# Optimization experiments

Hardware: AMD Instinct MI355X
Metric: run time of the kernel (lower is better)

Reference implementation:

```python
import jax, jax.numpy as jnp
import numpy as np

K_TOP = 2          # hardcoded k in MyAttentionFunction
S = 32             # hardcoded spatial size (interpolate to 32x32)
N = S * S          # 1024 patches (patch_size=1, stride=1 unfold)
NEG = jnp.float32(-1e30)  # stand-in for excluding columns from top-k


def setup_inputs() -> dict:
    key = jax.random.key(0)
    k1, k2, k3 = jax.random.split(key, 3)
    C = 4096
    generated = jax.random.normal(k1, (1, C, S, S), dtype=jnp.float32)
    known = jax.random.normal(k2, (1, C, S, S), dtype=jnp.float32)
    mask = jax.random.randint(k3, (1, 1, S, S), 0, 2).astype(jnp.float32)
    return {"generated": generated, "known": known, "mask": mask}


def _forward(generated, known, mask):
    C = generated.shape[1]
    # F.interpolate(mask, (32,32)) nearest, then flatten -> flag in {0,1}, shape (N,)
    flag = jax.image.resize(mask, (1, 1, S, S), method="nearest").reshape(N)
    # MyUnfold(x, 1, 1) == [1, N, C]; drop batch dim of 1.
    P = generated.reshape(C, N).T   # (N, C) patches of `generated`
    Kp = known.reshape(C, N).T      # (N, C) patches of `known`

    norm_p = jnp.sum(P * P, axis=-1)   # (N,)
    norm_k = jnp.sum(Kp * Kp, axis=-1)
    # Full cosine matrices; original restricts rows to flag==1 and columns to
    # flag==0 (cosine0) / flag==1 (cosine1) by extraction; we mask columns with
    # a very negative value so top-k returns the same values with GLOBAL indices
    # (which is exactly what the original reconstructs via nonzero()[indexes]).
    cos0 = (P @ Kp.T) / jnp.sqrt(norm_p[:, None] * norm_k[None, :])  # (N, N)
    cos1 = (P @ P.T) / jnp.sqrt(norm_p[:, None] * norm_p[None, :])
    cos0 = jnp.where(flag[None, :] == 0, cos0, NEG)
    cos1 = jnp.where(flag[None, :] == 1, cos1, NEG)

    w0, i0 = jax.lax.top_k(cos0, K_TOP)  # (N, k) values / global indices
    w1, i1 = jax.lax.top_k(cos1, K_TOP)

    m = flag                      # 1.0 on masked rows
    nm = jnp.sum(m)               # number of masked patches
    # weight means taken only over masked rows, then softmax (original uses
    # .item() + numpy softmax, i.e. detached constants).
    means = jnp.stack(
        [jnp.sum(w0[:, i] * m) / nm for i in range(K_TOP)]
        + [jnp.sum(w1[:, i] * m) / nm for i in range(K_TOP)]
    )
    weights = jax.lax.stop_gradient(jax.nn.softmax(means))  # (2k,)

    # The original builds dense 1024x1024 indicator matrices and bmm's them;
    # each indicator row for a masked patch is one-hot at its retrieved source,
    # so the bmm is just a gather into masked rows. The advanced-indexing quirk
    # ind[mask_idx, src_idx] (nonzero() pairs include a leading 0 column) also
    # unconditionally sets ind[0,0]=1; we reproduce that (set semantics: no
    # double count if row 0 already maps to column 0).
    rtn = jnp.zeros((N, C), dtype=generated.dtype)
    for i in range(2 * K_TOP):
        src = Kp if i < K_TOP else P
        cols = (i0 if i < K_TOP else i1)[:, i % K_TOP]  # (N,) global indices
        out_i = jnp.where(m[:, None] == 1, src[cols], 0.0)  # masked rows only
        dup = 1.0 - ((m[0] == 1) & (cols[0] == 0)).astype(src.dtype)
        out_i = out_i.at[0].add(src[0] * dup)  # spurious ind[0,0]=1 artifact
        rtn = rtn + weights[i] * out_i

    rtn = rtn.reshape(1, S, S, C).transpose(0, 3, 1, 2)  # (1, C, 32, 32)
    return jnp.concatenate([generated, known, rtn], axis=1)


def reference(generated, known, mask):
    return _forward(generated, known, mask)
```

## Files before the change

### kernel.cpp

```cpp
#include <hip/hip_runtime.h>
#include <hip/hip_bf16.h>
#include <math.h>

#define N_TOT 1024
#define C_DIM 4096
#define T_MARGIN 3e-4f

typedef __attribute__((ext_vector_type(8))) _Float16 half8;
typedef __attribute__((ext_vector_type(8))) unsigned short ushort8;
typedef __attribute__((ext_vector_type(8))) char schar8;
typedef __attribute__((ext_vector_type(4))) float floatx4;

__device__ inline unsigned short f2h(float v) {
    _Float16 h = (_Float16)v;
    return __builtin_bit_cast(unsigned short, h);
}
__device__ inline float h2f(unsigned short u) {
    return (float)__builtin_bit_cast(_Float16, u);
}
__device__ inline char lo_enc(float v, unsigned short h) {
    int e = (h >> 10) & 31;
    float lo = v - h2f(h);
    float q = rintf(lo * 240.0f * __uint_as_float((unsigned)(152 - e) << 23));
    q = fmaxf(-127.0f, fminf(127.0f, q));
    return (char)(int)q;
}
__device__ inline float lo_dec(char q, unsigned short h) {
    int e = (h >> 10) & 31;
    return (float)q * __uint_as_float((unsigned)(e + 102) << 23) * (1.0f / 240.0f);
}

__device__ inline void ins2(float v, int s, float& v1, int& s1, float& v2, int& s2) {
    if (v > v1 || (v == v1 && s < s1)) { v2 = v1; s2 = s1; v1 = v; s1 = s; }
    else if (v > v2 || (v == v2 && s < s2)) { v2 = v; s2 = s; }
}

__global__ __launch_bounds__(256) void split_norms(const float* __restrict__ G,
                                                   const float* __restrict__ Kn,
                                                   const float* __restrict__ flag,
                                                   unsigned short* __restrict__ Phi,
                                                   char* __restrict__ Plo,
                                                   unsigned short* __restrict__ Khi,
                                                   char* __restrict__ Klo,
                                                   float* __restrict__ normP,
                                                   float* __restrict__ normK,
                                                   int* __restrict__ colidx,
                                                   int* __restrict__ n0p) {
    const int z = blockIdx.z;
    const float* X = z ? Kn : G;
    unsigned short* Xhi = z ? Khi : Phi;
    char* Xlo = z ? Klo : Plo;
    float* normX = z ? normK : normP;

    __shared__ float tile[64 * 65];
    __shared__ float np[256];
    const int t  = threadIdx.x;
    const int c0 = blockIdx.x * 64;
    const int n0 = blockIdx.y * 64;

    float s2 = 0.0f;
    #pragma unroll
    for (int s = 0; s < 16; s++) {
        int c_loc = s * 4 + (t >> 6);
        int n_loc = t & 63;
        float v = X[(c0 + c_loc) * N_TOT + n0 + n_loc];
        tile[c_loc * 65 + n_loc] = v;
        s2 = fmaf(v, v, s2);
    }
    np[t] = s2;
    __syncthreads();

    if (t < 64) {
        float tot = np[t] + np[t + 64] + np[t + 128] + np[t + 192];
        atomicAdd(&normX[n0 + t], tot);
    }

    #pragma unroll
    for (int s = 0; s < 4; s++) {
        int n_loc = s * 16 + (t >> 4);
        int c4    = (t & 15) * 4;
        unsigned short h[4]; char l[4];
        #pragma unroll
        for (int e = 0; e < 4; e++) {
            float v = tile[(c4 + e) * 65 + n_loc];
            h[e] = f2h(v);
            l[e] = lo_enc(v, h[e]);
        }
        size_t base = (size_t)(n0 + n_loc) * C_DIM + c0 + c4;
        *(ushort4*)&Xhi[base] = make_ushort4(h[0], h[1], h[2], h[3]);
        *(char4*)&Xlo[base]   = make_char4(l[0], l[1], l[2], l[3]);
    }

    if (blockIdx.x == 0 && blockIdx.y == 0 && blockIdx.z == 0) {
        __shared__ int cz[256];
        __shared__ int co[256];
        float4 fv = *(const float4*)&flag[4 * t];
        int f[4] = {fv.x == 0.0f, fv.y == 0.0f, fv.z == 0.0f, fv.w == 0.0f};
        int nz = f[0] + f[1] + f[2] + f[3];
        cz[t] = nz; co[t] = 4 - nz;
        __syncthreads();
        for (int off = 1; off < 256; off <<= 1) {
            int vz = (t >= off) ? cz[t - off] : 0;
            int vo = (t >= off) ? co[t - off] : 0;
            __syncthreads();
            cz[t] += vz; co[t] += vo;
            __syncthreads();
        }
        const int fn0 = cz[255];
        int zs = cz[t] - nz;
        int os = fn0 + co[t] - (4 - nz);
        #pragma unroll
        for (int e = 0; e < 4; e++) {
            int j = 4 * t + e;
            if (f[e]) colidx[zs++] = j;
            else      colidx[os++] = j;
        }
        if (t == 0) *n0p = fn0;
    }
}

__global__ __launch_bounds__(256, 4) void gemm_coarse(const unsigned short* __restrict__ Phi,
                                                      const unsigned short* __restrict__ Khi,
                                                      const int* __restrict__ colidx,
                                                      const int* __restrict__ n0p,
                                                      float* __restrict__ dotPart) {
    __shared__ unsigned short sA[64 * 64];
    __shared__ unsigned short sB[128 * 64];

    const int t    = threadIdx.x;
    const int wave = t >> 6, lane = t & 63;
    const int wm   = wave >> 1, wn = wave & 1;
    const int quad = lane >> 4, lrow = lane & 15;
    const int ib = blockIdx.x * 64, jb = blockIdx.y * 128;
    const int bz = blockIdx.z;
    const int k_beg = bz * 512;
    const int n0 = *n0p;

    const int srow = t >> 3;
    const int g    = (t & 7) ^ (srow & 7);

    const unsigned short* gA[2];
    gA[0] = Phi + (size_t)(ib + srow) * C_DIM + g * 8;
    gA[1] = gA[0] + (size_t)32 * C_DIM;
    const unsigned short* gB[4];
    #pragma unroll
    for (int q = 0; q < 4; q++) {
        int s = jb + q * 32 + srow;
        int row = colidx[s];
        const unsigned short* src = (s < n0) ? Khi : Phi;
        gB[q] = src + (size_t)row * C_DIM + g * 8;
    }

    floatx4 acc[2][4] = {};

    for (int k0 = k_beg; k0 < k_beg + 512; k0 += 64) {
        #pragma unroll
        for (int q = 0; q < 2; q++)
            __builtin_amdgcn_global_load_lds(
                (const __attribute__((address_space(1))) void*)(gA[q] + k0),
                (__attribute__((address_space(3))) void*)((char*)sA + q * 4096 + t * 16), 16, 0, 0);
        #pragma unroll
        for (int q = 0; q < 4; q++)
            __builtin_amdgcn_global_load_lds(
                (const __attribute__((address_space(1))) void*)(gB[q] + k0),
                (__attribute__((address_space(3))) void*)((char*)sB + q * 4096 + t * 16), 16, 0, 0);
        __syncthreads();

        #pragma unroll
        for (int kk = 0; kk < 2; kk++) {
            const int gk = kk * 4 + quad;
            half8 a[2], b[4];
            #pragma unroll
            for (int ti = 0; ti < 2; ti++) {
                int m = wm * 32 + ti * 16 + lrow;
                a[ti] = *(const half8*)&sA[m * 64 + ((gk ^ (m & 7)) << 3)];
            }
            #pragma unroll
            for (int tj = 0; tj < 4; tj++) {
                int n = wn * 64 + tj * 16 + lrow;
                b[tj] = *(const half8*)&sB[n * 64 + ((gk ^ (n & 7)) << 3)];
            }
            #pragma unroll
            for (int ti = 0; ti < 2; ti++)
                #pragma unroll
                for (int tj = 0; tj < 4; tj++)
                    acc[ti][tj] = __builtin_amdgcn_mfma_f32_16x16x32_f16(a[ti], b[tj], acc[ti][tj], 0, 0, 0);
        }
        __syncthreads();
    }

    float* outp = dotPart + ((size_t)bz << 20);
    #pragma unroll
    for (int tj = 0; tj < 4; tj++) {
        int j = jb + wn * 64 + tj * 16 + lrow;
        #pragma unroll
        for (int ti = 0; ti < 2; ti++) {
            #pragma unroll
            for (int reg = 0; reg < 4; reg++) {
                int i = ib + wm * 32 + ti * 16 + quad * 4 + reg;
                outp[i * N_TOT + j] = acc[ti][tj][reg];
            }
        }
    }
}

__global__ __launch_bounds__(256) void topk_refine(const float* __restrict__ dotPart,
                                                   const unsigned short* __restrict__ Phi,
                                                   const char* __restrict__ Plo,
                                                   const unsigned short* __restrict__ Khi,
                                                   const char* __restrict__ Klo,
                                                   const float* __restrict__ normP,
                                                   const float* __restrict__ normK,
                                                   const int* __restrict__ colidx,
                                                   const int* __restrict__ n0p,
                                                   float* __restrict__ w01,
                                                   int* __restrict__ i01) {
    __shared__ float sAf[C_DIM];
    __shared__ float sr_v1[2][4], sr_v2[2][4];
    __shared__ int   sr_s1[2][4], sr_s2[2][4];
    __shared__ int   s_cnt[2];
    __shared__ int   s_cand[2][16];
    __shared__ float s_rcv[16];

    const int row = blockIdx.x;
    const int t   = threadIdx.x;
    const int wave = t >> 6, lane = t & 63;
    const int n0 = *n0p;
    const float nr = normP[row];

    if (t < 2) s_cnt[t] = 0;

    float4 dv = make_float4(0.f, 0.f, 0.f, 0.f);
    #pragma unroll
    for (int z = 0; z < 8; z++) {
        float4 p = *(const float4*)&dotPart[((size_t)z << 20) + (size_t)row * N_TOT + 4 * t];
        dv.x += p.x; dv.y += p.y; dv.z += p.z; dv.w += p.w;
    }

    float cv[4];
    #pragma unroll
    for (int e = 0; e < 4; e++) {
        int s = 4 * t + e;
        int gj = colidx[s];
        float nb = (s < n0) ? normK[gj] : normP[gj];
        float d  = (e == 0) ? dv.x : (e == 1) ? dv.y : (e == 2) ? dv.z : dv.w;
        cv[e] = d * rsqrtf(nr * nb);
    }

    #pragma unroll
    for (int zz = 0; zz < 2; zz++) {
        float v1 = -INFINITY, v2 = -INFINITY;
        int   s1 = 0x7FFFFFFF, s2 = 0x7FFFFFFF;
        #pragma unroll
        for (int e = 0; e < 4; e++) {
            int s = 4 * t + e;
            bool inz = zz ? (s >= n0) : (s < n0);
            if (inz) ins2(cv[e], s, v1, s1, v2, s2);
        }
        #pragma unroll
        for (int off = 32; off > 0; off >>= 1) {
            float o1 = __shfl_xor(v1, off); int q1 = __shfl_xor(s1, off);
            float o2 = __shfl_xor(v2, off); int q2 = __shfl_xor(s2, off);
            ins2(o1, q1, v1, s1, v2, s2);
            ins2(o2, q2, v1, s1, v2, s2);
        }
        if (lane == 0) {
            sr_v1[zz][wave] = v1; sr_s1[zz][wave] = s1;
            sr_v2[zz][wave] = v2; sr_s2[zz][wave] = s2;
        }
    }
    __syncthreads();

    float m1z[2], m2z[2]; int b1z[2], b2z[2];
    #pragma unroll
    for (int zz = 0; zz < 2; zz++) {
        float m1 = -INFINITY, m2 = -INFINITY;
        int   b1 = 0x7FFFFFFF, b2 = 0x7FFFFFFF;
        #pragma unroll
        for (int w = 0; w < 4; w++) {
            ins2(sr_v1[zz][w], sr_s1[zz][w], m1, b1, m2, b2);
            ins2(sr_v2[zz][w], sr_s2[zz][w], m1, b1, m2, b2);
        }
        m1z[zz] = m1; m2z[zz] = m2; b1z[zz] = b1; b2z[zz] = b2;
        const float thr = m2 - T_MARGIN;
        #pragma unroll
        for (int e = 0; e < 4; e++) {
            int s = 4 * t + e;
            bool inz = zz ? (s >= n0) : (s < n0);
            if (inz && cv[e] > thr) {
                int idx = atomicAdd(&s_cnt[zz], 1);
                if (idx < 16) s_cand[zz][idx] = s;
            }
        }
    }
    __syncthreads();

    bool need[2];
    #pragma unroll
    for (int zz = 0; zz < 2; zz++) {
        const int cnt = s_cnt[zz];
        const bool trusted = (cnt == 2) && (m1z[zz] - m2z[zz] > T_MARGIN);
        need[zz] = !trusted;
        if (trusted && t == 0) {
            int base = (zz * N_TOT + row) * 2;
            w01[base]     = m1z[zz];
            w01[base + 1] = m2z[zz];
            i01[base]     = colidx[b1z[zz]];
            i01[base + 1] = colidx[b2z[zz]];
        }
    }

    if (!need[0] && !need[1]) return;

    {
        const unsigned short* Ah = Phi + (size_t)row * C_DIM;
        const char*           Al = Plo + (size_t)row * C_DIM;
        #pragma unroll
        for (int s = 0; s < 2; s++) {
            int c = t * 16 + s * 8;
            ushort8 hb = *(const ushort8*)&Ah[c];
            schar8  lb = *(const schar8*)&Al[c];
            #pragma unroll
            for (int e = 0; e < 8; e++) sAf[c + e] = h2f(hb[e]) + lo_dec(lb[e], hb[e]);
        }
    }
    __syncthreads();

    const int grp = t >> 5, l32 = t & 31;
    #pragma unroll
    for (int zz = 0; zz < 2; zz++) {
        if (!need[zz]) continue;
        const int cnt = (s_cnt[zz] < 16) ? s_cnt[zz] : 16;
        #pragma unroll
        for (int p = 0; p < 2; p++) {
            if (p == 1 && cnt <= 8) break;
            const int q = grp + 8 * p;
            float acc = 0.0f;
            if (q < cnt) {
                const int cs = s_cand[zz][q];
                const int gj = colidx[cs];
                const unsigned short* bh_row = ((cs < n0) ? Khi : Phi) + (size_t)gj * C_DIM;
                const char*           bl_row = ((cs < n0) ? Klo : Plo) + (size_t)gj * C_DIM;
                #pragma unroll 4
                for (int it = 0; it < 16; it++) {
                    int c = it * 256 + l32 * 8;
                    ushort8 hb = *(const ushort8*)&bh_row[c];
                    schar8  lb = *(const schar8*)&bl_row[c];
                    #pragma unroll
                    for (int e = 0; e < 8; e++)
                        acc = fmaf(sAf[c + e], h2f(hb[e]) + lo_dec(lb[e], hb[e]), acc);
                }
            }
            #pragma unroll
            for (int off = 16; off > 0; off >>= 1) acc += __shfl_xor(acc, off);
            if (l32 == 0) s_rcv[q] = acc;
        }
        __syncthreads();

        if (t == 0) {
            float v1 = -INFINITY, v2 = -INFINITY;
            int   j1 = 0x7FFFFFFF, j2 = 0x7FFFFFFF;
            for (int q = 0; q < cnt; q++) {
                int cs = s_cand[zz][q];
                int gj = colidx[cs];
                float nb = (cs < n0) ? normK[gj] : normP[gj];
                float cvx = s_rcv[q] * rsqrtf(nr * nb);
                if (cvx > v1 || (cvx == v1 && gj < j1)) {
                    v2 = v1; j2 = j1; v1 = cvx; j1 = gj;
                } else if (cvx > v2 || (cvx == v2 && gj < j2)) {
                    v2 = cvx; j2 = gj;
                }
            }
            if (j1 == 0x7FFFFFFF) j1 = 0;
            if (j2 == 0x7FFFFFFF) j2 = j1;
            int base = (zz * N_TOT + row) * 2;
            w01[base]     = v1;
            w01[base + 1] = v2;
            i01[base]     = j1;
            i01[base + 1] = j2;
        }
        __syncthreads();
    }
}

__global__ __launch_bounds__(256) void output_kernel(const float* __restrict__ G,
                                                     const float* __restrict__ Kn,
                                                     const float* __restrict__ flag,
                                                     const float* __restrict__ w01,
                                                     const int* __restrict__ i01,
                                                     float* __restrict__ out) {
    __shared__ float red[5][4];
    __shared__ float wts[4];
    const int c  = blockIdx.x;
    const int t  = threadIdx.x;
    const int n4 = t * 4;

    float4 fv = *(const float4*)&flag[n4];
    const float fa[4] = {fv.x, fv.y, fv.z, fv.w};

    float pm[5] = {};
    #pragma unroll
    for (int e = 0; e < 4; e++) {
        int n = n4 + e;
        float m = fa[e];
        pm[0] += m;
        pm[1] += m * w01[n * 2 + 0];
        pm[2] += m * w01[n * 2 + 1];
        pm[3] += m * w01[2 * N_TOT + n * 2 + 0];
        pm[4] += m * w01[2 * N_TOT + n * 2 + 1];
    }
    #pragma unroll
    for (int i = 0; i < 5; i++)
        #pragma unroll
        for (int off = 32; off > 0; off >>= 1)
            pm[i] += __shfl_xor(pm[i], off);
    const int wave = t >> 6, lane = t & 63;
    if (lane == 0) {
        #pragma unroll
        for (int i = 0; i < 5; i++) red[i][wave] = pm[i];
    }
    __syncthreads();
    if (t == 0) {
        float tot[5];
        #pragma unroll
        for (int i = 0; i < 5; i++)
            tot[i] = red[i][0] + red[i][1] + red[i][2] + red[i][3];
        float inv = 1.0f / tot[0];
        float mv[4] = {tot[1] * inv, tot[2] * inv, tot[3] * inv, tot[4] * inv};
        float mx = fmaxf(fmaxf(mv[0], mv[1]), fmaxf(mv[2], mv[3]));
        float e[4], s = 0.0f;
        #pragma unroll
        for (int q = 0; q < 4; q++) { e[q] = expf(mv[q] - mx); s += e[q]; }
        #pragma unroll
        for (int q = 0; q < 4; q++) wts[q] = e[q] / s;
    }
    __syncthreads();
    const float w0 = wts[0], w1 = wts[1], w2 = wts[2], w3 = wts[3];

    float4 gv = *(const float4*)&G[c * N_TOT + n4];
    float4 kv = *(const float4*)&Kn[c * N_TOT + n4];
    *(float4*)&out[c * N_TOT + n4] = gv;
    *(float4*)&out[C_DIM * N_TOT + c * N_TOT + n4] = kv;

    float val[4];
    #pragma unroll
    for (int e = 0; e < 4; e++) {
        int n = n4 + e;
        float v = 0.0f;
        if (fa[e] == 1.0f) {
            int c00 = i01[n * 2 + 0];
            int c01 = i01[n * 2 + 1];
            int c10 = i01[2 * N_TOT + n * 2 + 0];
            int c11 = i01[2 * N_TOT + n * 2 + 1];
            v = w0 * Kn[c * N_TOT + c00] + w1 * Kn[c * N_TOT + c01]
              + w2 * G[c * N_TOT + c10]  + w3 * G[c * N_TOT + c11];
        }
        if (n == 0) {
            bool m0 = (flag[0] == 1.0f);
            int c00 = i01[0], c01 = i01[1];
            int c10 = i01[2 * N_TOT], c11 = i01[2 * N_TOT + 1];
            float kn0 = Kn[c * N_TOT];
            float g0  = G[c * N_TOT];
            if (!(m0 && c00 == 0)) v += w0 * kn0;
            if (!(m0 && c01 == 0)) v += w1 * kn0;
            if (!(m0 && c10 == 0)) v += w2 * g0;
            if (!(m0 && c11 == 0)) v += w3 * g0;
        }
        val[e] = v;
    }
    *(float4*)&out[2 * C_DIM * N_TOT + c * N_TOT + n4] =
        make_float4(val[0], val[1], val[2], val[3]);
}

extern "C" void kernel_launch(void* const* d_in, const int* in_sizes, int n_in,
                              void* d_out, int out_size, void* d_ws, size_t ws_size,
                              hipStream_t stream) {
    const float* G    = (const float*)d_in[0];
    const float* Kn   = (const float*)d_in[1];
    const float* flag = (const float*)d_in[2];
    float* out = (float*)d_out;

    char* p = (char*)d_ws;
    unsigned short* Phi = (unsigned short*)p;  p += (size_t)N_TOT * C_DIM * 2;
    unsigned short* Khi = (unsigned short*)p;  p += (size_t)N_TOT * C_DIM * 2;
    char* Plo = p;                             p += (size_t)N_TOT * C_DIM;
    char* Klo = p;                             p += (size_t)N_TOT * C_DIM;
    float* dotPart = (float*)p;                p += (size_t)8 * N_TOT * N_TOT * 4;
    float* normP  = (float*)p;                 p += N_TOT * 4;
    float* normK  = (float*)p;                 p += N_TOT * 4;
    float* w01    = (float*)p;                 p += 4 * N_TOT * 4;
    int*   i01    = (int*)p;                   p += 4 * N_TOT * 4;
    int*   colidx = (int*)p;                   p += N_TOT * 4;
    int*   n0p    = (int*)p;

    hipMemsetAsync(normP, 0, 2 * N_TOT * sizeof(float), stream);

    split_norms<<<dim3(64, 16, 2), 256, 0, stream>>>(G, Kn, flag, Phi, Plo, Khi, Klo,
                                                     normP, normK, colidx, n0p);
    gemm_coarse<<<dim3(16, 8, 8), 256, 0, stream>>>(Phi, Khi, colidx, n0p, dotPart);
    topk_refine<<<1024, 256, 0, stream>>>(dotPart, Phi, Plo, Khi, Klo,
                                          normP, normK, colidx, n0p, w01, i01);
    output_kernel<<<4096, 256, 0, stream>>>(G, Kn, flag, w01, i01, out);
}
```

Before: 174.5 us.

## Split top-k into scan pass plus worklist-driven refine kernel; precompute softmax means

```diff
diff --git a/kernel.cpp b/kernel.cpp
--- a/kernel.cpp
+++ b/kernel.cpp
@@ -204,23 +204,23 @@
     }
 }
 
-__global__ __launch_bounds__(256) void topk_refine(const float* __restrict__ dotPart,
-                                                   const unsigned short* __restrict__ Phi,
-                                                   const char* __restrict__ Plo,
-                                                   const unsigned short* __restrict__ Khi,
-                                                   const char* __restrict__ Klo,
-                                                   const float* __restrict__ normP,
-                                                   const float* __restrict__ normK,
-                                                   const int* __restrict__ colidx,
-                                                   const int* __restrict__ n0p,
-                                                   float* __restrict__ w01,
-                                                   int* __restrict__ i01) {
-    __shared__ float sAf[C_DIM];
+__global__ __launch_bounds__(256) void topk_pass1(const float* __restrict__ dotPart,
+                                                  const float* __restrict__ flag,
+                                                  const float* __restrict__ normP,
+                                                  const float* __restrict__ normK,
+                                                  const int* __restrict__ colidx,
+                                                  const int* __restrict__ n0p,
+                                                  float* __restrict__ w01,
+                                                  int* __restrict__ i01,
+                                                  float* __restrict__ meanAcc,
+                                                  int* __restrict__ wlCount,
+                                                  int* __restrict__ wl_hdr,
+                                                  int* __restrict__ wl_cand) {
     __shared__ float sr_v1[2][4], sr_v2[2][4];
     __shared__ int   sr_s1[2][4], sr_s2[2][4];
     __shared__ int   s_cnt[2];
     __shared__ int   s_cand[2][16];
-    __shared__ float s_rcv[16];
+    __shared__ int   s_slot[2];
 
     const int row = blockIdx.x;
     const int t   = threadIdx.x;
@@ -295,50 +295,95 @@
     }
     __syncthreads();
 
-    bool need[2];
+    const bool fr = (flag[row] == 1.0f);
+    bool need[2]; int cntz[2];
     #pragma unroll
     for (int zz = 0; zz < 2; zz++) {
-        const int cnt = s_cnt[zz];
-        const bool trusted = (cnt == 2) && (m1z[zz] - m2z[zz] > T_MARGIN);
+        const int cnt = min(s_cnt[zz], 16);
+        cntz[zz] = cnt;
+        const bool trusted = (s_cnt[zz] == 2) && (m1z[zz] - m2z[zz] > T_MARGIN);
         need[zz] = !trusted;
-        if (trusted && t == 0) {
-            int base = (zz * N_TOT + row) * 2;
-            w01[base]     = m1z[zz];
-            w01[base + 1] = m2z[zz];
-            i01[base]     = colidx[b1z[zz]];
-            i01[base + 1] = colidx[b2z[zz]];
-        }
-    }
-
-    if (!need[0] && !need[1]) return;
-
-    {
-        const unsigned short* Ah = Phi + (size_t)row * C_DIM;
-        const char*           Al = Plo + (size_t)row * C_DIM;
-        #pragma unroll
-        for (int s = 0; s < 2; s++) {
-            int c = t * 16 + s * 8;
-            ushort8 hb = *(const ushort8*)&Ah[c];
-            schar8  lb = *(const schar8*)&Al[c];
+        if (t == 0) {
+            if (trusted) {
+                int base = (zz * N_TOT + row) * 2;
+                w01[base]     = m1z[zz];
+                w01[base + 1] = m2z[zz];
+                i01[base]     = colidx[b1z[zz]];
+                i01[base + 1] = colidx[b2z[zz]];
+                if (fr) {
+                    atomicAdd(&meanAcc[zz * 2],     m1z[zz]);
+                    atomicAdd(&meanAcc[zz * 2 + 1], m2z[zz]);
+                }
+            } else {
+                int slot = atomicAdd(wlCount, 1);
+                s_slot[zz] = slot;
+                wl_hdr[slot] = row | (zz << 16) | (cnt << 20);
+            }
+        }
+    }
+    __syncthreads();
+
+    #pragma unroll
+    for (int zz = 0; zz < 2; zz++)
+        if (need[zz] && t < cntz[zz])
+            wl_cand[s_slot[zz] * 16 + t] = s_cand[zz][t];
+}
+
+__global__ __launch_bounds__(256) void refine2(const unsigned short* __restrict__ Phi,
+                                               const char* __restrict__ Plo,
+                                               const unsigned short* __restrict__ Khi,
+                                               const char* __restrict__ Klo,
+                                               const float* __restrict__ normP,
+                                               const float* __restrict__ normK,
+                                               const int* __restrict__ colidx,
+                                               const int* __restrict__ n0p,
+                                               const float* __restrict__ flag,
+                                               const int* __restrict__ wlCount,
+                                               const int* __restrict__ wl_hdr,
+                                               const int* __restrict__ wl_cand,
+                                               float* __restrict__ w01,
+                                               int* __restrict__ i01,
+                                               float* __restrict__ meanAcc) {
+    __shared__ float sAf[C_DIM];
+    __shared__ float s_rcv[16];
+    __shared__ int   s_rcj[16];
+
+    const int t   = threadIdx.x;
+    const int grp = t >> 5, l32 = t & 31;
+    const int total = *wlCount;
+    const int n0 = *n0p;
+
+    for (int item = blockIdx.x; item < total; item += gridDim.x) {
+        const int hdr = wl_hdr[item];
+        const int row = hdr & 0xFFFF;
+        const int zz  = (hdr >> 16) & 1;
+        const int cnt = hdr >> 20;
+        const float nr = normP[row];
+
+        {
+            const unsigned short* Ah = Phi + (size_t)row * C_DIM;
+            const char*           Al = Plo + (size_t)row * C_DIM;
             #pragma unroll
-            for (int e = 0; e < 8; e++) sAf[c + e] = h2f(hb[e]) + lo_dec(lb[e], hb[e]);
-        }
-    }
-    __syncthreads();
-
-    const int grp = t >> 5, l32 = t & 31;
-    #pragma unroll
-    for (int zz = 0; zz < 2; zz++) {
-        if (!need[zz]) continue;
-        const int cnt = (s_cnt[zz] < 16) ? s_cnt[zz] : 16;
+            for (int s = 0; s < 2; s++) {
+                int c = t * 16 + s * 8;
+                ushort8 hb = *(const ushort8*)&Ah[c];
+                schar8  lb = *(const schar8*)&Al[c];
+                #pragma unroll
+                for (int e = 0; e < 8; e++) sAf[c + e] = h2f(hb[e]) + lo_dec(lb[e], hb[e]);
+            }
+        }
+        __syncthreads();
+
         #pragma unroll
         for (int p = 0; p < 2; p++) {
             if (p == 1 && cnt <= 8) break;
             const int q = grp + 8 * p;
             float acc = 0.0f;
+            int gj = 0; float nb = 1.0f;
             if (q < cnt) {
-                const int cs = s_cand[zz][q];
-                const int gj = colidx[cs];
+                const int cs = wl_cand[item * 16 + q];
+                gj = colidx[cs];
+                nb = (cs < n0) ? normK[gj] : normP[gj];
                 const unsigned short* bh_row = ((cs < n0) ? Khi : Phi) + (size_t)gj * C_DIM;
                 const char*           bl_row = ((cs < n0) ? Klo : Plo) + (size_t)gj * C_DIM;
                 #pragma unroll 4
@@ -353,7 +398,10 @@
             }
             #pragma unroll
             for (int off = 16; off > 0; off >>= 1) acc += __shfl_xor(acc, off);
-            if (l32 == 0) s_rcv[q] = acc;
+            if (l32 == 0 && q < cnt) {
+                s_rcv[q] = acc * rsqrtf(nr * nb);
+                s_rcj[q] = gj;
+            }
         }
         __syncthreads();
 
@@ -361,14 +409,12 @@
             float v1 = -INFINITY, v2 = -INFINITY;
             int   j1 = 0x7FFFFFFF, j2 = 0x7FFFFFFF;
             for (int q = 0; q < cnt; q++) {
-                int cs = s_cand[zz][q];
-                int gj = colidx[cs];
-                float nb = (cs < n0) ? normK[gj] : normP[gj];
-                float cvx = s_rcv[q] * rsqrtf(nr * nb);
-                if (cvx > v1 || (cvx == v1 && gj < j1)) {
-                    v2 = v1; j2 = j1; v1 = cvx; j1 = gj;
-                } else if (cvx > v2 || (cvx == v2 && gj < j2)) {
-                    v2 = cvx; j2 = gj;
+                float cvx = s_rcv[q];
+                int   j   = s_rcj[q];
+                if (cvx > v1 || (cvx == v1 && j < j1)) {
+                    v2 = v1; j2 = j1; v1 = cvx; j1 = j;
+                } else if (cvx > v2 || (cvx == v2 && j < j2)) {
+                    v2 = cvx; j2 = j;
                 }
             }
             if (j1 == 0x7FFFFFFF) j1 = 0;
@@ -378,6 +424,10 @@
             w01[base + 1] = v2;
             i01[base]     = j1;
             i01[base + 1] = j2;
+            if (flag[row] == 1.0f) {
+                atomicAdd(&meanAcc[zz * 2],     v1);
+                atomicAdd(&meanAcc[zz * 2 + 1], v2);
+            }
         }
         __syncthreads();
     }
@@ -388,54 +438,30 @@
                                                      const float* __restrict__ flag,
                                                      const float* __restrict__ w01,
                                                      const int* __restrict__ i01,
+                                                     const float* __restrict__ meanAcc,
+                                                     const int* __restrict__ n0p,
                                                      float* __restrict__ out) {
-    __shared__ float red[5][4];
     __shared__ float wts[4];
     const int c  = blockIdx.x;
     const int t  = threadIdx.x;
     const int n4 = t * 4;
 
+    if (t == 0) {
+        float inv = 1.0f / (float)(N_TOT - *n0p);
+        float mv[4] = {meanAcc[0] * inv, meanAcc[1] * inv,
+                       meanAcc[2] * inv, meanAcc[3] * inv};
+        float mx = fmaxf(fmaxf(mv[0], mv[1]), fmaxf(mv[2], mv[3]));
+        float e[4], s = 0.0f;
+        #pragma unroll
+        for (int q = 0; q < 4; q++) { e[q] = expf(mv[q] - mx); s += e[q]; }
+        #pragma unroll
+        for (int q = 0; q < 4; q++) wts[q] = e[q] / s;
+    }
+    __syncthreads();
+    const float w0 = wts[0], w1 = wts[1], w2 = wts[2], w3 = wts[3];
+
     float4 fv = *(const float4*)&flag[n4];
     const float fa[4] = {fv.x, fv.y, fv.z, fv.w};
-
-    float pm[5] = {};
-    #pragma unroll
-    for (int e = 0; e < 4; e++) {
-        int n = n4 + e;
-        float m = fa[e];
-        pm[0] += m;
-        pm[1] += m * w01[n * 2 + 0];
-        pm[2] += m * w01[n * 2 + 1];
-        pm[3] += m * w01[2 * N_TOT + n * 2 + 0];
-        pm[4] += m * w01[2 * N_TOT + n * 2 + 1];
-    }
-    #pragma unroll
-    for (int i = 0; i < 5; i++)
-        #pragma unroll
-        for (int off = 32; off > 0; off >>= 1)
-            pm[i] += __shfl_xor(pm[i], off);
-    const int wave = t >> 6, lane = t & 63;
-    if (lane == 0) {
-        #pragma unroll
-        for (int i = 0; i < 5; i++) red[i][wave] = pm[i];
-    }
-    __syncthreads();
-    if (t == 0) {
-        float tot[5];
-        #pragma unroll
-        for (int i = 0; i < 5; i++)
-            tot[i] = red[i][0] + red[i][1] + red[i][2] + red[i][3];
-        float inv = 1.0f / tot[0];
-        float mv[4] = {tot[1] * inv, tot[2] * inv, tot[3] * inv, tot[4] * inv};
-        float mx = fmaxf(fmaxf(mv[0], mv[1]), fmaxf(mv[2], mv[3]));
-        float e[4], s = 0.0f;
-        #pragma unroll
-        for (int q = 0; q < 4; q++) { e[q] = expf(mv[q] - mx); s += e[q]; }
-        #pragma unroll
-        for (int q = 0; q < 4; q++) wts[q] = e[q] / s;
-    }
-    __syncthreads();
-    const float w0 = wts[0], w1 = wts[1], w2 = wts[2], w3 = wts[3];
 
     float4 gv = *(const float4*)&G[c * N_TOT + n4];
     float4 kv = *(const float4*)&Kn[c * N_TOT + n4];
@@ -486,19 +512,25 @@
     char* Plo = p;                             p += (size_t)N_TOT * C_DIM;
     char* Klo = p;                             p += (size_t)N_TOT * C_DIM;
     float* dotPart = (float*)p;                p += (size_t)8 * N_TOT * N_TOT * 4;
-    float* normP  = (float*)p;                 p += N_TOT * 4;
-    float* normK  = (float*)p;                 p += N_TOT * 4;
-    float* w01    = (float*)p;                 p += 4 * N_TOT * 4;
-    int*   i01    = (int*)p;                   p += 4 * N_TOT * 4;
-    int*   colidx = (int*)p;                   p += N_TOT * 4;
-    int*   n0p    = (int*)p;
-
-    hipMemsetAsync(normP, 0, 2 * N_TOT * sizeof(float), stream);
+    float* normP   = (float*)p;                p += N_TOT * 4;
+    float* normK   = (float*)p;                p += N_TOT * 4;
+    float* meanAcc = (float*)p;                p += 4 * 4;
+    int*   wlCount = (int*)p;                  p += 16;
+    float* w01     = (float*)p;                p += 4 * N_TOT * 4;
+    int*   i01     = (int*)p;                  p += 4 * N_TOT * 4;
+    int*   colidx  = (int*)p;                  p += N_TOT * 4;
+    int*   n0p     = (int*)p;                  p += 16;
+    int*   wl_hdr  = (int*)p;                  p += 2048 * 4;
+    int*   wl_cand = (int*)p;
+
+    hipMemsetAsync(normP, 0, 2 * N_TOT * sizeof(float) + 32, stream);
 
     split_norms<<<dim3(64, 16, 2), 256, 0, stream>>>(G, Kn, flag, Phi, Plo, Khi, Klo,
                                                      normP, normK, colidx, n0p);
     gemm_coarse<<<dim3(16, 8, 8), 256, 0, stream>>>(Phi, Khi, colidx, n0p, dotPart);
-    topk_refine<<<1024, 256, 0, stream>>>(dotPart, Phi, Plo, Khi, Klo,
-                                          normP, normK, colidx, n0p, w01, i01);
-    output_kernel<<<4096, 256, 0, stream>>>(G, Kn, flag, w01, i01, out);
-}
+    topk_pass1<<<1024, 256, 0, stream>>>(dotPart, flag, normP, normK, colidx, n0p,
+                                         w01, i01, meanAcc, wlCount, wl_hdr, wl_cand);
+    refine2<<<1024, 256, 0, stream>>>(Phi, Plo, Khi, Klo, normP, normK, colidx, n0p,
+                                      flag, wlCount, wl_hdr, wl_cand, w01, i01, meanAcc);
+    output_kernel<<<4096, 256, 0, stream>>>(G, Kn, flag, w01, i01, meanAcc, n0p, out);
+}
```

Measured after the change: 195.0 us. 1.12x slower.
